# Optimization experiments

Measured on AMD Instinct MI355X. Metric: run time of the kernel, lower is better.

The kernel has to match this reference:

```python
import jax, jax.numpy as jnp
import numpy as np

N_NODES = 65536
N_EDGES = N_NODES * 16
NEG_SLOPE = 0.2


def setup_inputs() -> dict:
    key = jax.random.key(0)
    ks = jax.random.split(key, 32)
    x = jax.random.normal(ks[0], (N_NODES, 336), dtype=jnp.float32)
    ei = jax.random.randint(ks[1], (2, N_EDGES), 0, N_NODES)
    src, dst = ei[0], ei[1]
    dst = jnp.where(src == dst, (dst + 1) % N_NODES, dst)  # no pre-existing self-loops
    edge_index = jnp.stack([src, dst])
    batch = jnp.arange(N_NODES) // 8

    def mk(k, shape, fan_in):
        return jax.random.normal(k, shape, dtype=jnp.float32) * (1.0 / np.sqrt(fan_in))

    conv_dims = [(336, 125), (250, 75), (150, 50), (100, 30)]
    H = 2
    p = {}
    ki = 2
    for i, (cin, cout) in enumerate(conv_dims, 1):
        p[f"W{i}"] = mk(ks[ki], (cin, H * cout), cin); ki += 1
        p[f"as{i}"] = mk(ks[ki], (H, cout), cout); ki += 1
        p[f"ad{i}"] = mk(ks[ki], (H, cout), cout); ki += 1
        p[f"b{i}"] = jnp.zeros((H * cout,), dtype=jnp.float32)
    lin_dims = [(480, 200), (200, 100), (100, 100), (100, 29)]
    for i, (cin, cout) in enumerate(lin_dims, 1):
        p[f"lw{i}"] = mk(ks[ki], (cin, cout), cin); ki += 1
        p[f"lb{i}"] = jnp.zeros((cout,), dtype=jnp.float32)
    return {"x": x, "edge_index": edge_index, "batch": batch, **p}


def gat_conv(x, src, dst, W, a_src, a_dst, bias):
    # PyG GATConv (concat=True): gather -> LeakyReLU score -> segment softmax over dst -> scatter-add
    N = x.shape[0]
    H, C = a_src.shape
    h = (x @ W).reshape(N, H, C)                      # [N,H,C]
    al_s = jnp.sum(h * a_src, axis=-1)                # [N,H]
    al_d = jnp.sum(h * a_dst, axis=-1)
    e = jax.nn.leaky_relu(al_s[src] + al_d[dst], NEG_SLOPE)  # [E,H]
    m = jax.ops.segment_max(e, dst, num_segments=N)   # [N,H]
    m = jnp.where(jnp.isfinite(m), m, 0.0)
    ex = jnp.exp(e - m[dst])
    den = jax.ops.segment_sum(ex, dst, num_segments=N)
    alpha = ex / den[dst]                             # [E,H]
    out = jax.ops.segment_sum(alpha[:, :, None] * h[src], dst, num_segments=N)
    return out.reshape(N, H * C) + bias


def reference(x, edge_index, batch,
              W1, as1, ad1, b1, W2, as2, ad2, b2,
              W3, as3, ad3, b3, W4, as4, ad4, b4,
              lw1, lb1, lw2, lb2, lw3, lb3, lw4, lb4):
    N = x.shape[0]
    loops = jnp.arange(N)
    src = jnp.concatenate([edge_index[0], loops])  # add self-loops (PyG default)
    dst = jnp.concatenate([edge_index[1], loops])
    h = jax.nn.relu(gat_conv(x, src, dst, W1, as1, ad1, b1))
    h = jax.nn.relu(gat_conv(h, src, dst, W2, as2, ad2, b2))
    h = jax.nn.relu(gat_conv(h, src, dst, W3, as3, ad3, b3))
    h = jax.nn.relu(gat_conv(h, src, dst, W4, as4, ad4, b4))
    h = h.reshape(-1, 480)                         # 8 nodes per graph * 60 feats
    h = jax.nn.relu(h @ lw1 + lb1)
    h = jax.nn.relu(h @ lw2 + lb2)
    h = jax.nn.relu(h @ lw3 + lb3)
    return h @ lw4 + lb4
```

## Files before the change

kernel.cpp:

```cpp
#include <hip/hip_runtime.h>
#include <hip/hip_bf16.h>
#include <stdint.h>

#define N_NODES 65536
#define N_EDGES (N_NODES * 16)
#define NEG_SLOPE 0.2f

typedef short bf16x8 __attribute__((ext_vector_type(8)));
typedef float f32x4 __attribute__((ext_vector_type(4)));
typedef unsigned int u32x2 __attribute__((ext_vector_type(2)));
typedef _Float16 f16x4 __attribute__((ext_vector_type(4)));

__device__ __forceinline__ unsigned short f2bf(float f) {
    unsigned u = __float_as_uint(f);
    u += 0x7fffu + ((u >> 16) & 1u);
    return (unsigned short)(u >> 16);
}
__device__ __forceinline__ float bf2f(unsigned short h) {
    return __uint_as_float(((unsigned)h) << 16);
}
__device__ __forceinline__ unsigned short f2h(float f) {
    _Float16 h = (_Float16)f;
    union { _Float16 h; unsigned short u; } cv; cv.h = h; return cv.u;
}
__device__ __forceinline__ float rl_f(float v, int lane) {
    return __int_as_float(__builtin_amdgcn_readlane(__float_as_int(v), lane));
}
__device__ __forceinline__ void load_lds16(const void* g, void* l) {
    __builtin_amdgcn_global_load_lds(
        (const __attribute__((address_space(1))) unsigned int*)g,
        (__attribute__((address_space(3))) unsigned int*)l, 16, 0, 0);
}
__device__ __forceinline__ void nt_store_us4(unsigned short* p, ushort4 v) {
    u32x2 d;
    d.x = (unsigned)v.x | ((unsigned)v.y << 16);
    d.y = (unsigned)v.z | ((unsigned)v.w << 16);
    __builtin_nontemporal_store(d, (u32x2*)p);
}

template<int TN>
__global__ __launch_bounds__(256) void gemm_mfma(
    const float* __restrict__ A32, int KA,
    const unsigned short* __restrict__ Ahi, const unsigned short* __restrict__ Alo,
    int lda, int Kp,
    const unsigned short* __restrict__ Bhi, const unsigned short* __restrict__ Blo,
    unsigned short* __restrict__ C16,
    int ldc, int Nw,
    const float* __restrict__ asrc, const float* __restrict__ adst,
    float* __restrict__ alS, float* __restrict__ alD, int Cal, int HCal)
{
    constexpr int NI = TN / 32;
    __shared__ unsigned short sAhi[128 * 32], sAlo[128 * 32];
    __shared__ unsigned short sBhi[TN * 32],  sBlo[TN * 32];
    __shared__ float sAl[128][2][4];
    const int tid = threadIdx.x;
    const int wave = tid >> 6, lane = tid & 63;
    const int row0 = blockIdx.y * 128;
    const int col0 = blockIdx.x * TN;
    const int wm = (wave & 1) * 64, wn = (wave >> 1) * (TN / 2);
    const int mlane = lane & 15, q = lane >> 4;

    f32x4 acc[4][NI];
#pragma unroll
    for (int a = 0; a < 4; ++a)
#pragma unroll
        for (int b = 0; b < NI; ++b) acc[a][b] = (f32x4){0.f, 0.f, 0.f, 0.f};

    for (int k0 = 0; k0 < Kp; k0 += 32) {
        __syncthreads();
        if (A32) {
            const int r = tid >> 1, cbase = (tid & 1) * 16;
            const float* Ap = A32 + (size_t)(row0 + r) * lda;
#pragma unroll
            for (int j = 0; j < 4; ++j) {
                int kc = k0 + cbase + j * 4;
                float4 v = make_float4(0.f, 0.f, 0.f, 0.f);
                if (kc < KA) v = *(const float4*)(Ap + kc);
                ushort4 h, l;
                h.x = f2bf(v.x); l.x = f2bf(v.x - bf2f(h.x));
                h.y = f2bf(v.y); l.y = f2bf(v.y - bf2f(h.y));
                h.z = f2bf(v.z); l.z = f2bf(v.z - bf2f(h.z));
                h.w = f2bf(v.w); l.w = f2bf(v.w - bf2f(h.w));
                *(ushort4*)(sAhi + r * 32 + cbase + j * 4) = h;
                *(ushort4*)(sAlo + r * 32 + cbase + j * 4) = l;
            }
        } else {
#pragma unroll
            for (int cc = 0; cc < 2; ++cc) {
                int c = wave * 2 + cc;
                int r = c * 16 + (lane >> 2);
                size_t goff = (size_t)(row0 + r) * lda + k0 + (lane & 3) * 8;
                load_lds16(Ahi + goff, sAhi + c * 512);
                load_lds16(Alo + goff, sAlo + c * 512);
            }
        }
        {
#pragma unroll
            for (int cc = 0; cc < TN / 64; ++cc) {
                int c = wave * (TN / 64) + cc;
                int r = c * 16 + (lane >> 2);
                size_t goff = (size_t)(col0 + r) * Kp + k0 + (lane & 3) * 8;
                load_lds16(Bhi + goff, sBhi + c * 512);
                load_lds16(Blo + goff, sBlo + c * 512);
            }
        }
        __syncthreads();

        bf16x8 ah[4], al[4], bh[NI], bl[NI];
#pragma unroll
        for (int mi = 0; mi < 4; ++mi) {
            int m = wm + mi * 16 + mlane;
            ah[mi] = *(const bf16x8*)(sAhi + m * 32 + q * 8);
            al[mi] = *(const bf16x8*)(sAlo + m * 32 + q * 8);
        }
#pragma unroll
        for (int ni = 0; ni < NI; ++ni) {
            int n = wn + ni * 16 + mlane;
            bh[ni] = *(const bf16x8*)(sBhi + n * 32 + q * 8);
            bl[ni] = *(const bf16x8*)(sBlo + n * 32 + q * 8);
        }
#pragma unroll
        for (int mi = 0; mi < 4; ++mi)
#pragma unroll
            for (int ni = 0; ni < NI; ++ni) {
                acc[mi][ni] = __builtin_amdgcn_mfma_f32_16x16x32_bf16(ah[mi], bh[ni], acc[mi][ni], 0, 0, 0);
                acc[mi][ni] = __builtin_amdgcn_mfma_f32_16x16x32_bf16(al[mi], bh[ni], acc[mi][ni], 0, 0, 0);
                acc[mi][ni] = __builtin_amdgcn_mfma_f32_16x16x32_bf16(ah[mi], bl[ni], acc[mi][ni], 0, 0, 0);
            }
    }

#pragma unroll
    for (int ni = 0; ni < NI; ++ni) {
        int col = col0 + wn + ni * 16 + mlane;
        if (col >= Nw) continue;
#pragma unroll
        for (int mi = 0; mi < 4; ++mi) {
#pragma unroll
            for (int reg = 0; reg < 4; ++reg) {
                int row = row0 + wm + mi * 16 + q * 4 + reg;
                C16[(size_t)row * ldc + col] = f2h(acc[mi][ni][reg]);
            }
        }
    }

    if (asrc) {
        float asv[NI], adv[NI];
        bool head0[NI];
#pragma unroll
        for (int ni = 0; ni < NI; ++ni) {
            int col = col0 + wn + ni * 16 + mlane;
            bool valid = col < HCal;
            head0[ni] = col < Cal;
            asv[ni] = valid ? asrc[col] : 0.f;
            adv[ni] = valid ? adst[col] : 0.f;
        }
#pragma unroll
        for (int mi = 0; mi < 4; ++mi) {
#pragma unroll
            for (int reg = 0; reg < 4; ++reg) {
                float s0 = 0.f, s1 = 0.f, d0 = 0.f, d1 = 0.f;
#pragma unroll
                for (int ni = 0; ni < NI; ++ni) {
                    float v = acc[mi][ni][reg];
                    if (head0[ni]) { s0 += v * asv[ni]; d0 += v * adv[ni]; }
                    else           { s1 += v * asv[ni]; d1 += v * adv[ni]; }
                }
#pragma unroll
                for (int off = 1; off < 16; off <<= 1) {
                    s0 += __shfl_xor(s0, off); s1 += __shfl_xor(s1, off);
                    d0 += __shfl_xor(d0, off); d1 += __shfl_xor(d1, off);
                }
                if (mlane == 0) {
                    int rl = wm + mi * 16 + q * 4 + reg;
                    int slot = wave >> 1;
                    sAl[rl][slot][0] = s0; sAl[rl][slot][1] = s1;
                    sAl[rl][slot][2] = d0; sAl[rl][slot][3] = d1;
                }
            }
        }
        __syncthreads();
        if (tid < 128) {
            int row = row0 + tid;
            float v0 = sAl[tid][0][0] + sAl[tid][1][0];
            float v1 = sAl[tid][0][1] + sAl[tid][1][1];
            float v2 = sAl[tid][0][2] + sAl[tid][1][2];
            float v3 = sAl[tid][0][3] + sAl[tid][1][3];
            atomicAdd(&alS[row * 2 + 0], v0);
            atomicAdd(&alS[row * 2 + 1], v1);
            atomicAdd(&alD[row * 2 + 0], v2);
            atomicAdd(&alD[row * 2 + 1], v3);
        }
    }
}

template<int NI>
__device__ __forceinline__ void mlp_layer(
    const unsigned short* aHi, const unsigned short* aLo, int ldaS, int K,
    const unsigned short* __restrict__ Bhi, const unsigned short* __restrict__ Blo,
    int Kp,
    unsigned short* sBh, unsigned short* sBl,
    const float* __restrict__ bias, int Nbias, int colBase,
    unsigned short* oHi, unsigned short* oLo, int ldo, int Nstore,
    float* __restrict__ gOut, int row0, int relu,
    int wave, int lane)
{
    const int mlane = lane & 15, q = lane >> 4;
    const int wm = (wave & 1) * 16;
    const int wn = (wave >> 1) * (NI * 16);
    f32x4 acc[NI];
#pragma unroll
    for (int b = 0; b < NI; ++b) acc[b] = (f32x4){0.f, 0.f, 0.f, 0.f};

    for (int k0 = 0; k0 < K; k0 += 32) {
        __syncthreads();
        for (int c = wave; c < NI * 2; c += 4) {
            int r = c * 16 + (lane >> 2);
            size_t goff = (size_t)r * Kp + k0 + (lane & 3) * 8;
            load_lds16(Bhi + goff, sBh + c * 512);
            load_lds16(Blo + goff, sBl + c * 512);
        }
        __syncthreads();

        bf16x8 ah, al, bh[NI], bl[NI];
        ah = *(const bf16x8*)(aHi + (wm + mlane) * ldaS + k0 + q * 8);
        al = *(const bf16x8*)(aLo + (wm + mlane) * ldaS + k0 + q * 8);
#pragma unroll
        for (int ni = 0; ni < NI; ++ni) {
            int n = wn + ni * 16 + mlane;
            bh[ni] = *(const bf16x8*)(sBh + n * 32 + q * 8);
            bl[ni] = *(const bf16x8*)(sBl + n * 32 + q * 8);
        }
#pragma unroll
        for (int ni = 0; ni < NI; ++ni) {
            acc[ni] = __builtin_amdgcn_mfma_f32_16x16x32_bf16(ah, bh[ni], acc[ni], 0, 0, 0);
            acc[ni] = __builtin_amdgcn_mfma_f32_16x16x32_bf16(al, bh[ni], acc[ni], 0, 0, 0);
            acc[ni] = __builtin_amdgcn_mfma_f32_16x16x32_bf16(ah, bl[ni], acc[ni], 0, 0, 0);
        }
    }
    __syncthreads();

#pragma unroll
    for (int ni = 0; ni < NI; ++ni) {
        int colg = colBase + wn + ni * 16 + mlane;
        float bv = (colg < Nbias) ? bias[colg] : 0.f;
#pragma unroll
        for (int reg = 0; reg < 4; ++reg) {
            int row = wm + q * 4 + reg;
            float v = acc[ni][reg] + bv;
            if (relu) v = fmaxf(v, 0.f);
            if (gOut) {
                if (colg < 29) gOut[(size_t)(row0 + row) * 29 + colg] = v;
            } else if (colg < Nstore) {
                unsigned short h = f2bf(v);
                oHi[row * ldo + colg] = h;
                oLo[row * ldo + colg] = f2bf(v - bf2f(h));
            }
        }
    }
}

__global__ __launch_bounds__(256) void mlp_fused(
    const unsigned short* __restrict__ actHi, const unsigned short* __restrict__ actLo,
    const unsigned short* __restrict__ L1h, const unsigned short* __restrict__ L1l,
    const unsigned short* __restrict__ L2h, const unsigned short* __restrict__ L2l,
    const unsigned short* __restrict__ L3h, const unsigned short* __restrict__ L3l,
    const unsigned short* __restrict__ L4h, const unsigned short* __restrict__ L4l,
    const float* __restrict__ B1, const float* __restrict__ B2,
    const float* __restrict__ B3, const float* __restrict__ B4,
    float* __restrict__ out)
{
    __shared__ unsigned short b1h[32 * 224], b1l[32 * 224];
    __shared__ unsigned short b2h[32 * 128], b2l[32 * 128];
    __shared__ unsigned short sAh[32 * 32],  sAl[32 * 32];
    __shared__ unsigned short sBh[128 * 32], sBl[128 * 32];
    const int tid = threadIdx.x;
    const int wave = tid >> 6, lane = tid & 63;
    const int row0 = blockIdx.x * 32;
    const int mlane = lane & 15, q = lane >> 4;
    const int wm = (wave & 1) * 16;
    const int wn = (wave >> 1) * 64;

    for (int nt = 0; nt < 2; ++nt) {
        const unsigned short* Bh = L1h + (size_t)nt * 128 * 512;
        const unsigned short* Bl = L1l + (size_t)nt * 128 * 512;
        f32x4 acc[4];
#pragma unroll
        for (int b = 0; b < 4; ++b) acc[b] = (f32x4){0.f, 0.f, 0.f, 0.f};
        for (int k0 = 0; k0 < 512; k0 += 32) {
            __syncthreads();
            for (int c = wave; c < 2; c += 4) {
                int r = c * 16 + (lane >> 2);
                size_t goff = (size_t)(row0 + r) * 512 + k0 + (lane & 3) * 8;
                load_lds16(actHi + goff, sAh + c * 512);
                load_lds16(actLo + goff, sAl + c * 512);
            }
            for (int c = wave; c < 8; c += 4) {
                int r = c * 16 + (lane >> 2);
                size_t goff = (size_t)r * 512 + k0 + (lane & 3) * 8;
                load_lds16(Bh + goff, sBh + c * 512);
                load_lds16(Bl + goff, sBl + c * 512);
            }
            __syncthreads();
            bf16x8 ah = *(const bf16x8*)(sAh + (wm + mlane) * 32 + q * 8);
            bf16x8 al = *(const bf16x8*)(sAl + (wm + mlane) * 32 + q * 8);
#pragma unroll
            for (int ni = 0; ni < 4; ++ni) {
                int n = wn + ni * 16 + mlane;
                bf16x8 bh = *(const bf16x8*)(sBh + n * 32 + q * 8);
                bf16x8 bl = *(const bf16x8*)(sBl + n * 32 + q * 8);
                acc[ni] = __builtin_amdgcn_mfma_f32_16x16x32_bf16(ah, bh, acc[ni], 0, 0, 0);
                acc[ni] = __builtin_amdgcn_mfma_f32_16x16x32_bf16(al, bh, acc[ni], 0, 0, 0);
                acc[ni] = __builtin_amdgcn_mfma_f32_16x16x32_bf16(ah, bl, acc[ni], 0, 0, 0);
            }
        }
        __syncthreads();
#pragma unroll
        for (int ni = 0; ni < 4; ++ni) {
            int colg = nt * 128 + wn + ni * 16 + mlane;
            float bv = (colg < 200) ? B1[colg] : 0.f;
#pragma unroll
            for (int reg = 0; reg < 4; ++reg) {
                int row = wm + q * 4 + reg;
                float v = fmaxf(acc[ni][reg] + bv, 0.f);
                if (colg < 224) {
                    unsigned short h = f2bf(v);
                    b1h[row * 224 + colg] = h;
                    b1l[row * 224 + colg] = f2bf(v - bf2f(h));
                }
            }
        }
    }
    __syncthreads();

    mlp_layer<4>(b1h, b1l, 224, 224, L2h, L2l, 224, sBh, sBl,
                 B2, 100, 0, b2h, b2l, 128, 128, nullptr, 0, 1, wave, lane);
    __syncthreads();
    mlp_layer<4>(b2h, b2l, 128, 128, L3h, L3l, 128, sBh, sBl,
                 B3, 100, 0, b1h, b1l, 128, 128, nullptr, 0, 1, wave, lane);
    __syncthreads();
    mlp_layer<2>(b1h, b1l, 128, 128, L4h, L4l, 128, sBh, sBl,
                 B4, 29, 0, nullptr, nullptr, 0, 0, out, row0, 0, wave, lane);
}

struct WtJob {
    const float* W; unsigned short* Whi; unsigned short* Wlo;
    int K, N, Kp, remap, nb0;
};
struct WtJobs { WtJob j[8]; };

__global__ void wt_decomp_all(WtJobs jobs)
{
    int b = blockIdx.x;
    int idx = 0;
#pragma unroll
    for (int i = 1; i < 8; ++i)
        if (b >= jobs.j[i].nb0) idx = i;
    WtJob jb = jobs.j[idx];
    int n = b - jb.nb0;
    for (int k = threadIdx.x; k < jb.Kp; k += 256) {
        int ks = k, valid = 1;
        if (jb.remap) {
            int bb = k >> 6, r = k & 63;
            if (r < 60) ks = bb * 60 + r; else valid = 0;
        }
        float v = 0.f;
        if (valid && ks < jb.K && n < jb.N) v = jb.W[(size_t)ks * jb.N + n];
        unsigned short h = f2bf(v);
        jb.Whi[(size_t)n * jb.Kp + k] = h;
        jb.Wlo[(size_t)n * jb.Kp + k] = f2bf(v - bf2f(h));
    }
}

template<int LPE>
__global__ __launch_bounds__(256) void gat_gather_fused(
    const unsigned short* __restrict__ h16,
    const float* __restrict__ al_s, const float* __restrict__ al_d,
    const int* __restrict__ indptr, const unsigned short* __restrict__ csr_src,
    const float* __restrict__ bias,
    unsigned short* __restrict__ outHi, unsigned short* __restrict__ outLo,
    int ldo, int Nn, int C, int HC, int HCpad)
{
    constexpr int G = 64 / LPE;
    const int wave = threadIdx.x >> 6, lane = threadIdx.x & 63;
    const int i = blockIdx.x * 4 + wave;
    if (i >= Nn) return;
    const int start = indptr[i], end = indptr[i + 1];
    const int deg = end - start;
    const float ad0 = al_d[2 * i], ad1 = al_d[2 * i + 1];

    const int l = lane % LPE;
    const int g = lane / LPE;
    const int ch4 = l * 4;
    const bool chA = ch4 < HCpad;
    const bool c0 = (ch4 + 0) < C, c1 = (ch4 + 1) < C,
               c2 = (ch4 + 2) < C, c3 = (ch4 + 3) < C;
    float a0 = 0.f, a1 = 0.f, a2 = 0.f, a3 = 0.f;

    if (deg <= 64) {
        const int jW = start + lane;
        const bool have = jW < end;
        int ps = 0;
        float e0r = 0.f, e1r = 0.f;
        if (have) {
            ps = csr_src[jW];
            float2 as = *(const float2*)(al_s + 2 * ps);
            e0r = as.x + ad0; e0r = e0r > 0.f ? e0r : NEG_SLOPE * e0r;
            e1r = as.y + ad1; e1r = e1r > 0.f ? e1r : NEG_SLOPE * e1r;
        }
        float m0 = have ? e0r : -1e30f;
        float m1 = have ? e1r : -1e30f;
#pragma unroll
        for (int off = 32; off; off >>= 1) {
            m0 = fmaxf(m0, __shfl_xor(m0, off));
            m1 = fmaxf(m1, __shfl_xor(m1, off));
        }
        float n0 = have ? __expf(e0r - m0) : 0.f;
        float n1 = have ? __expf(e1r - m1) : 0.f;
        float den0 = n0, den1 = n1;
#pragma unroll
        for (int off = 32; off; off >>= 1) {
            den0 += __shfl_xor(den0, off);
            den1 += __shfl_xor(den1, off);
        }
        const float pw0 = n0 * (1.f / den0);
        const float pw1 = n1 * (1.f / den1);

        if constexpr (G == 1) {
            for (int u = 0; u < deg; ++u) {
                float w0 = rl_f(pw0, u);
                float w1 = rl_f(pw1, u);
                int s = __builtin_amdgcn_readlane(ps, u);
                float hx = 0.f, hy = 0.f, hz = 0.f, hw = 0.f;
                if (chA) {
                    f16x4 hv = *(const f16x4*)(h16 + (size_t)s * HCpad + ch4);
                    hx = (float)hv[0]; hy = (float)hv[1];
                    hz = (float)hv[2]; hw = (float)hv[3];
                }
                a0 = fmaf(c0 ? w0 : w1, hx, a0);
                a1 = fmaf(c1 ? w0 : w1, hy, a1);
                a2 = fmaf(c2 ? w0 : w1, hz, a2);
                a3 = fmaf(c3 ? w0 : w1, hw, a3);
            }
        } else {
            const int nit = (deg + G - 1) / G;
            for (int u = 0; u < nit; ++u) {
                int idx = u * G + g;
                float w0 = __shfl(pw0, idx);
                float w1 = __shfl(pw1, idx);
                int s = __shfl(ps, idx);
                float hx = 0.f, hy = 0.f, hz = 0.f, hw = 0.f;
                if (chA) {
                    f16x4 hv = *(const f16x4*)(h16 + (size_t)s * HCpad + ch4);
                    hx = (float)hv[0]; hy = (float)hv[1];
                    hz = (float)hv[2]; hw = (float)hv[3];
                }
                a0 = fmaf(c0 ? w0 : w1, hx, a0);
                a1 = fmaf(c1 ? w0 : w1, hy, a1);
                a2 = fmaf(c2 ? w0 : w1, hz, a2);
                a3 = fmaf(c3 ? w0 : w1, hw, a3);
            }
        }
    } else {
        float m0 = -1e30f, m1 = -1e30f, den0 = 0.f, den1 = 0.f;
        for (int j = start + lane; j < end; j += 64) {
            int s = csr_src[j];
            float2 as = *(const float2*)(al_s + 2 * s);
            float e0 = as.x + ad0; e0 = e0 > 0.f ? e0 : NEG_SLOPE * e0;
            float e1 = as.y + ad1; e1 = e1 > 0.f ? e1 : NEG_SLOPE * e1;
            float n0 = fmaxf(m0, e0);
            den0 = den0 * __expf(m0 - n0) + __expf(e0 - n0);
            m0 = n0;
            float n1 = fmaxf(m1, e1);
            den1 = den1 * __expf(m1 - n1) + __expf(e1 - n1);
            m1 = n1;
        }
#pragma unroll
        for (int off = 32; off; off >>= 1) {
            float mo0 = __shfl_xor(m0, off), do0 = __shfl_xor(den0, off);
            float n0 = fmaxf(m0, mo0);
            den0 = den0 * __expf(m0 - n0) + do0 * __expf(mo0 - n0);
            m0 = n0;
            float mo1 = __shfl_xor(m1, off), do1 = __shfl_xor(den1, off);
            float n1 = fmaxf(m1, mo1);
            den1 = den1 * __expf(m1 - n1) + do1 * __expf(mo1 - n1);
            m1 = n1;
        }
        const float inv0 = 1.f / den0, inv1 = 1.f / den1;

        for (int jb = start; jb < end; jb += 64) {
            int jW = jb + lane;
            float pw0 = 0.f, pw1 = 0.f;
            int ps = 0;
            if (jW < end) {
                ps = csr_src[jW];
                float2 as = *(const float2*)(al_s + 2 * ps);
                float e0 = as.x + ad0; e0 = e0 > 0.f ? e0 : NEG_SLOPE * e0;
                float e1 = as.y + ad1; e1 = e1 > 0.f ? e1 : NEG_SLOPE * e1;
                pw0 = __expf(e0 - m0) * inv0;
                pw1 = __expf(e1 - m1) * inv1;
            }
            int nedge = end - jb; if (nedge > 64) nedge = 64;
            int nit = (nedge + G - 1) / G;
            for (int u = 0; u < nit; ++u) {
                int idx = u * G + g;
                float w0 = __shfl(pw0, idx);
                float w1 = __shfl(pw1, idx);
                int s = __shfl(ps, idx);
                float hx = 0.f, hy = 0.f, hz = 0.f, hw = 0.f;
                if (chA) {
                    f16x4 hv = *(const f16x4*)(h16 + (size_t)s * HCpad + ch4);
                    hx = (float)hv[0]; hy = (float)hv[1];
                    hz = (float)hv[2]; hw = (float)hv[3];
                }
                a0 = fmaf(c0 ? w0 : w1, hx, a0);
                a1 = fmaf(c1 ? w0 : w1, hy, a1);
                a2 = fmaf(c2 ? w0 : w1, hz, a2);
                a3 = fmaf(c3 ? w0 : w1, hw, a3);
            }
        }
    }

#pragma unroll
    for (int off = LPE; off < 64; off <<= 1) {
        a0 += __shfl_xor(a0, off);
        a1 += __shfl_xor(a1, off);
        a2 += __shfl_xor(a2, off);
        a3 += __shfl_xor(a3, off);
    }
    if (g == 0 && chA) {
        float bx = (ch4 + 0 < HC) ? bias[ch4 + 0] : 0.f;
        float by = (ch4 + 1 < HC) ? bias[ch4 + 1] : 0.f;
        float bz = (ch4 + 2 < HC) ? bias[ch4 + 2] : 0.f;
        float bw = (ch4 + 3 < HC) ? bias[ch4 + 3] : 0.f;
        float v0 = fmaxf(a0 + bx, 0.f);
        float v1 = fmaxf(a1 + by, 0.f);
        float v2 = fmaxf(a2 + bz, 0.f);
        float v3 = fmaxf(a3 + bw, 0.f);
        ushort4 h, lo;
        h.x = f2bf(v0); lo.x = f2bf(v0 - bf2f(h.x));
        h.y = f2bf(v1); lo.y = f2bf(v1 - bf2f(h.y));
        h.z = f2bf(v2); lo.z = f2bf(v2 - bf2f(h.z));
        h.w = f2bf(v3); lo.w = f2bf(v3 - bf2f(h.w));
        nt_store_us4(outHi + (size_t)i * ldo + ch4, h);
        nt_store_us4(outLo + (size_t)i * ldo + ch4, lo);
    }
    for (int z = HCpad + lane * 4; z < ldo; z += 256) {
        ushort4 zz; zz.x = zz.y = zz.z = zz.w = 0;
        *(ushort4*)(outHi + (size_t)i * ldo + z) = zz;
        *(ushort4*)(outLo + (size_t)i * ldo + z) = zz;
    }
}

__global__ void hist_self_k(const int* __restrict__ dst, int E,
                            int* __restrict__ counts, int n)
{
    int gid = blockIdx.x * blockDim.x + threadIdx.x;
    if (gid < E) atomicAdd(&counts[dst[gid]], 1);
    else if (gid < E + n) atomicAdd(&counts[gid - E], 1);
}

__global__ void scan_block_k(const int* __restrict__ in, int* __restrict__ out,
                             int* __restrict__ bsum, int n)
{
    __shared__ int sh[256];
    int gid = blockIdx.x * 256 + threadIdx.x;
    int v = (gid < n) ? in[gid] : 0;
    sh[threadIdx.x] = v;
    __syncthreads();
    for (int off = 1; off < 256; off <<= 1) {
        int t = (threadIdx.x >= off) ? sh[threadIdx.x - off] : 0;
        __syncthreads();
        sh[threadIdx.x] += t;
        __syncthreads();
    }
    int incl = sh[threadIdx.x];
    if (gid < n) out[gid] = incl - v;
    if (threadIdx.x == 255) bsum[blockIdx.x] = incl;
}

__global__ void scan_tops_k(const int* __restrict__ bsum, int* __restrict__ boff)
{
    __shared__ int sh[256];
    int v = bsum[threadIdx.x];
    sh[threadIdx.x] = v;
    __syncthreads();
    for (int off = 1; off < 256; off <<= 1) {
        int t = (threadIdx.x >= off) ? sh[threadIdx.x - off] : 0;
        __syncthreads();
        sh[threadIdx.x] += t;
        __syncthreads();
    }
    boff[threadIdx.x] = sh[threadIdx.x] - v;
}

__global__ void scan_add_k(int* __restrict__ indptr, const int* __restrict__ boff,
                           int n, int Etot)
{
    int gid = blockIdx.x * 256 + threadIdx.x;
    if (gid < n) indptr[gid] += boff[blockIdx.x];
    if (gid == 0) indptr[n] = Etot;
}

__global__ void fill_all_k(const int* __restrict__ src, const int* __restrict__ dst,
                           int E, const int* __restrict__ indptr,
                           int* __restrict__ cursor,
                           unsigned short* __restrict__ csr_src, int n)
{
    int gid = blockIdx.x * blockDim.x + threadIdx.x;
    if (gid < E) {
        int d = dst[gid];
        int pos = atomicAdd(&cursor[d], 1);
        csr_src[indptr[d] + pos] = (unsigned short)src[gid];
    } else if (gid < E + n) {
        int i = gid - E;
        int pos = atomicAdd(&cursor[i], 1);
        csr_src[indptr[i] + pos] = (unsigned short)i;
    }
}

extern "C" void kernel_launch(void* const* d_in, const int* in_sizes, int n_in,
                              void* d_out, int out_size, void* d_ws, size_t ws_size,
                              hipStream_t stream)
{
    (void)in_sizes; (void)n_in; (void)out_size; (void)ws_size;
    const int N = N_NODES;
    const int E = N_EDGES;
    const int Etot = E + N;

    const float* x = (const float*)d_in[0];
    const int* ei = (const int*)d_in[1];
    const float* Wc[4] = {(const float*)d_in[3], (const float*)d_in[7],
                          (const float*)d_in[11], (const float*)d_in[15]};
    const float* AS[4] = {(const float*)d_in[4], (const float*)d_in[8],
                          (const float*)d_in[12], (const float*)d_in[16]};
    const float* AD[4] = {(const float*)d_in[5], (const float*)d_in[9],
                          (const float*)d_in[13], (const float*)d_in[17]};
    const float* Bc[4] = {(const float*)d_in[6], (const float*)d_in[10],
                          (const float*)d_in[14], (const float*)d_in[18]};
    const float* LW[4] = {(const float*)d_in[19], (const float*)d_in[21],
                          (const float*)d_in[23], (const float*)d_in[25]};
    const float* LB[4] = {(const float*)d_in[20], (const float*)d_in[22],
                          (const float*)d_in[24], (const float*)d_in[26]};

    char* w = (char*)d_ws;
    auto alloc = [&](size_t bytes) -> char* {
        char* p = w; w += (bytes + 255) & ~(size_t)255; return p;
    };
    unsigned short* bufC16 = (unsigned short*)alloc((size_t)N * 256 * 2);
    unsigned short* actHi = (unsigned short*)alloc((size_t)N * 256 * 2);
    unsigned short* actLo = (unsigned short*)alloc((size_t)N * 256 * 2);
    unsigned short* csr = (unsigned short*)alloc((size_t)Etot * 2);
    float* alSD = (float*)alloc((size_t)N * 4 * 4 * 4 + (size_t)N * 2 * 4);
    int* cnt2   = (int*)(alSD + (size_t)N * 16);
    int* counts = cnt2;
    int* cursor = cnt2 + N;
    int* indptr = (int*)alloc((size_t)(N + 8) * 4);
    int* bsum   = (int*)alloc(1024);
    int* boff   = (int*)alloc(1024);

    const int KpConv[4] = {352, 256, 160, 128};
    const int NpConv[4] = {256, 192, 128, 64};
    const int KpLin[4]  = {512, 224, 128, 128};
    const int NpLin[4]  = {256, 128, 128, 64};
    unsigned short *WtHi[4], *WtLo[4], *LtHi[4], *LtLo[4];
    for (int l = 0; l < 4; ++l) {
        WtHi[l] = (unsigned short*)alloc((size_t)NpConv[l] * KpConv[l] * 2);
        WtLo[l] = (unsigned short*)alloc((size_t)NpConv[l] * KpConv[l] * 2);
    }
    for (int l = 0; l < 4; ++l) {
        LtHi[l] = (unsigned short*)alloc((size_t)NpLin[l] * KpLin[l] * 2);
        LtLo[l] = (unsigned short*)alloc((size_t)NpLin[l] * KpLin[l] * 2);
    }

    const int* esrc = ei;
    const int* edst = ei + E;

    hipMemsetAsync(alSD, 0, (size_t)N * 4 * 4 * 4 + (size_t)N * 2 * 4, stream);
    hist_self_k<<<(E + N) / 256, 256, 0, stream>>>(edst, E, counts, N);
    scan_block_k<<<N / 256, 256, 0, stream>>>(counts, indptr, bsum, N);
    scan_tops_k<<<1, 256, 0, stream>>>(bsum, boff);
    scan_add_k<<<N / 256, 256, 0, stream>>>(indptr, boff, N, Etot);
    fill_all_k<<<(E + N) / 256, 256, 0, stream>>>(esrc, edst, E, indptr, cursor, csr, N);

    const int Kc[4] = {336, 250, 150, 100}, Nc[4] = {250, 150, 100, 60};
    const int Kl[4] = {480, 200, 100, 100}, Nl[4] = {200, 100, 100, 29};
    WtJobs jobs;
    int nb = 0;
    for (int l = 0; l < 4; ++l) {
        jobs.j[l] = {Wc[l], WtHi[l], WtLo[l], Kc[l], Nc[l], KpConv[l], 0, nb};
        nb += NpConv[l];
    }
    for (int l = 0; l < 4; ++l) {
        jobs.j[4 + l] = {LW[l], LtHi[l], LtLo[l], Kl[l], Nl[l], KpLin[l],
                         l == 0 ? 1 : 0, nb};
        nb += NpLin[l];
    }
    wt_decomp_all<<<nb, 256, 0, stream>>>(jobs);

    const int HCp[4]  = {256, 152, 100, 60};
    const int ldoA[4] = {256, 160, 128, 64};
    const int ldaA[4] = {336, 256, 160, 128};
    for (int l = 0; l < 4; ++l) {
        int C = Nc[l] / 2, HC = Nc[l];
        float* alS = alSD + (size_t)l * N * 4;
        float* alD = alS + (size_t)N * 2;
        if (l == 0) {
            gemm_mfma<128><<<dim3(2, N / 128), 256, 0, stream>>>(
                x, 336, nullptr, nullptr, 336, 352,
                WtHi[0], WtLo[0],
                bufC16, HCp[0], HCp[0],
                AS[0], AD[0], alS, alD, C, HC);
        } else if (l == 1) {
            gemm_mfma<64><<<dim3(3, N / 128), 256, 0, stream>>>(
                nullptr, 0, actHi, actLo, ldaA[1], KpConv[1],
                WtHi[1], WtLo[1],
                bufC16, HCp[1], HCp[1],
                AS[1], AD[1], alS, alD, C, HC);
        } else if (l == 2) {
            gemm_mfma<128><<<dim3(1, N / 128), 256, 0, stream>>>(
                nullptr, 0, actHi, actLo, ldaA[2], KpConv[2],
                WtHi[2], WtLo[2],
                bufC16, HCp[2], HCp[2],
                AS[2], AD[2], alS, alD, C, HC);
        } else {
            gemm_mfma<64><<<dim3(1, N / 128), 256, 0, stream>>>(
                nullptr, 0, actHi, actLo, ldaA[3], KpConv[3],
                WtHi[3], WtLo[3],
                bufC16, HCp[3], HCp[3],
                AS[3], AD[3], alS, alD, C, HC);
        }
        if (l == 0) {
            gat_gather_fused<64><<<N / 4, 256, 0, stream>>>(
                bufC16, alS, alD, indptr, csr, Bc[0],
                actHi, actLo, ldoA[0], N, C, HC, HCp[0]);
        } else if (l == 1) {
            gat_gather_fused<64><<<N / 4, 256, 0, stream>>>(
                bufC16, alS, alD, indptr, csr, Bc[1],
                actHi, actLo, ldoA[1], N, C, HC, HCp[1]);
        } else if (l == 2) {
            gat_gather_fused<32><<<N / 4, 256, 0, stream>>>(
                bufC16, alS, alD, indptr, csr, Bc[2],
                actHi, actLo, ldoA[2], N, C, HC, HCp[2]);
        } else {
            gat_gather_fused<16><<<N / 4, 256, 0, stream>>>(
                bufC16, alS, alD, indptr, csr, Bc[3],
                actHi, actLo, ldoA[3], N, C, HC, HCp[3]);
        }
    }

    mlp_fused<<<8192 / 32, 256, 0, stream>>>(
        actHi, actLo,
        LtHi[0], LtLo[0], LtHi[1], LtLo[1],
        LtHi[2], LtLo[2], LtHi[3], LtLo[3],
        LB[0], LB[1], LB[2], LB[3],
        (float*)d_out);
}
```

Measured before the change: 813.3 us.

## Pad each attention head to aligned column blocks and unroll gather loops

Each head's channels are now laid out in a padded block (e.g. 125→128), and the weight-decomposition kernel remaps weight rows and columns to match. With this layout every 4-channel group in the gather kernel belongs to a single head, so one weight select replaces four per-element selects. The edge loops are rounded up to a multiple of four and unrolled by four, relying on zero weights for the padded edges. This adds index-remapping logic and slightly wider padded buffers, and leans on the padded entries reading as zero.

New measurement: 838.1 us. +3.0%, slower.

```diff
diff --git a/kernel.cpp b/kernel.cpp
--- a/kernel.cpp
+++ b/kernel.cpp
@@ -47,7 +47,7 @@
     unsigned short* __restrict__ C16,
     int ldc, int Nw,
     const float* __restrict__ asrc, const float* __restrict__ adst,
-    float* __restrict__ alS, float* __restrict__ alD, int Cal, int HCal)
+    float* __restrict__ alS, float* __restrict__ alD, int Cal, int Pal)
 {
     constexpr int NI = TN / 32;
     __shared__ unsigned short sAhi[128 * 32], sAlo[128 * 32];
@@ -149,10 +149,13 @@
 #pragma unroll
         for (int ni = 0; ni < NI; ++ni) {
             int col = col0 + wn + ni * 16 + mlane;
-            bool valid = col < HCal;
-            head0[ni] = col < Cal;
-            asv[ni] = valid ? asrc[col] : 0.f;
-            adv[ni] = valid ? adst[col] : 0.f;
+            int hd = col >= Pal;
+            int idc = hd ? col - Pal : col;
+            bool valid = idc < Cal;
+            head0[ni] = !hd;
+            int borig = hd ? Cal + idc : idc;
+            asv[ni] = valid ? asrc[borig] : 0.f;
+            adv[ni] = valid ? adst[borig] : 0.f;
         }
 #pragma unroll
         for (int mi = 0; mi < 4; ++mi) {
@@ -344,7 +347,7 @@
 
 struct WtJob {
     const float* W; unsigned short* Whi; unsigned short* Wlo;
-    int K, N, Kp, remap, nb0;
+    int N, Kp, K, nb0, Cn, Pn, Ck, Pk, kblk;
 };
 struct WtJobs { WtJob j[8]; };
 
@@ -357,14 +360,30 @@
         if (b >= jobs.j[i].nb0) idx = i;
     WtJob jb = jobs.j[idx];
     int n = b - jb.nb0;
+    int norig = n; bool nvalid;
+    if (jb.Pn) {
+        int hn = n >= jb.Pn;
+        int r = hn ? n - jb.Pn : n;
+        nvalid = r < jb.Cn;
+        norig = hn ? jb.Cn + r : r;
+    } else {
+        nvalid = n < jb.N;
+    }
     for (int k = threadIdx.x; k < jb.Kp; k += 256) {
-        int ks = k, valid = 1;
-        if (jb.remap) {
-            int bb = k >> 6, r = k & 63;
-            if (r < 60) ks = bb * 60 + r; else valid = 0;
+        int ks; bool kvalid;
+        if (jb.Pk) {
+            int node = k / jb.kblk;
+            int r = k - node * jb.kblk;
+            int rr, off;
+            if (r < jb.Pk) { rr = r; off = 0; kvalid = rr < jb.Ck; }
+            else if (r < 2 * jb.Pk) { rr = r - jb.Pk; off = jb.Ck; kvalid = rr < jb.Ck; }
+            else { rr = 0; off = 0; kvalid = false; }
+            ks = node * (2 * jb.Ck) + off + rr;
+        } else {
+            ks = k; kvalid = k < jb.K;
         }
         float v = 0.f;
-        if (valid && ks < jb.K && n < jb.N) v = jb.W[(size_t)ks * jb.N + n];
+        if (nvalid && kvalid) v = jb.W[(size_t)ks * jb.N + norig];
         unsigned short h = f2bf(v);
         jb.Whi[(size_t)n * jb.Kp + k] = h;
         jb.Wlo[(size_t)n * jb.Kp + k] = f2bf(v - bf2f(h));
@@ -378,7 +397,7 @@
     const int* __restrict__ indptr, const unsigned short* __restrict__ csr_src,
     const float* __restrict__ bias,
     unsigned short* __restrict__ outHi, unsigned short* __restrict__ outLo,
-    int ldo, int Nn, int C, int HC, int HCpad)
+    int ldo, int Nn, int C, int P, int HCpad)
 {
     constexpr int G = 64 / LPE;
     const int wave = threadIdx.x >> 6, lane = threadIdx.x & 63;
@@ -392,8 +411,7 @@
     const int g = lane / LPE;
     const int ch4 = l * 4;
     const bool chA = ch4 < HCpad;
-    const bool c0 = (ch4 + 0) < C, c1 = (ch4 + 1) < C,
-               c2 = (ch4 + 2) < C, c3 = (ch4 + 3) < C;
+    const bool hd1 = ch4 >= P;
     float a0 = 0.f, a1 = 0.f, a2 = 0.f, a3 = 0.f;
 
     if (deg <= 64) {
@@ -426,9 +444,12 @@
         const float pw1 = n1 * (1.f / den1);
 
         if constexpr (G == 1) {
-            for (int u = 0; u < deg; ++u) {
+            const int dr = (deg + 3) & ~3;
+#pragma unroll 4
+            for (int u = 0; u < dr; ++u) {
                 float w0 = rl_f(pw0, u);
                 float w1 = rl_f(pw1, u);
+                float w = hd1 ? w1 : w0;
                 int s = __builtin_amdgcn_readlane(ps, u);
                 float hx = 0.f, hy = 0.f, hz = 0.f, hw = 0.f;
                 if (chA) {
@@ -436,17 +457,20 @@
                     hx = (float)hv[0]; hy = (float)hv[1];
                     hz = (float)hv[2]; hw = (float)hv[3];
                 }
-                a0 = fmaf(c0 ? w0 : w1, hx, a0);
-                a1 = fmaf(c1 ? w0 : w1, hy, a1);
-                a2 = fmaf(c2 ? w0 : w1, hz, a2);
-                a3 = fmaf(c3 ? w0 : w1, hw, a3);
+                a0 = fmaf(w, hx, a0);
+                a1 = fmaf(w, hy, a1);
+                a2 = fmaf(w, hz, a2);
+                a3 = fmaf(w, hw, a3);
             }
         } else {
             const int nit = (deg + G - 1) / G;
-            for (int u = 0; u < nit; ++u) {
+            const int nit4 = (nit + 3) & ~3;
+#pragma unroll 4
+            for (int u = 0; u < nit4; ++u) {
                 int idx = u * G + g;
                 float w0 = __shfl(pw0, idx);
                 float w1 = __shfl(pw1, idx);
+                float w = hd1 ? w1 : w0;
                 int s = __shfl(ps, idx);
                 float hx = 0.f, hy = 0.f, hz = 0.f, hw = 0.f;
                 if (chA) {
@@ -454,10 +478,10 @@
                     hx = (float)hv[0]; hy = (float)hv[1];
                     hz = (float)hv[2]; hw = (float)hv[3];
                 }
-                a0 = fmaf(c0 ? w0 : w1, hx, a0);
-                a1 = fmaf(c1 ? w0 : w1, hy, a1);
-                a2 = fmaf(c2 ? w0 : w1, hz, a2);
-                a3 = fmaf(c3 ? w0 : w1, hw, a3);
+                a0 = fmaf(w, hx, a0);
+                a1 = fmaf(w, hy, a1);
+                a2 = fmaf(w, hz, a2);
+                a3 = fmaf(w, hw, a3);
             }
         }
     } else {
@@ -505,6 +529,7 @@
                 int idx = u * G + g;
                 float w0 = __shfl(pw0, idx);
                 float w1 = __shfl(pw1, idx);
+                float w = hd1 ? w1 : w0;
                 int s = __shfl(ps, idx);
                 float hx = 0.f, hy = 0.f, hz = 0.f, hw = 0.f;
                 if (chA) {
@@ -512,10 +537,10 @@
                     hx = (float)hv[0]; hy = (float)hv[1];
                     hz = (float)hv[2]; hw = (float)hv[3];
                 }
-                a0 = fmaf(c0 ? w0 : w1, hx, a0);
-                a1 = fmaf(c1 ? w0 : w1, hy, a1);
-                a2 = fmaf(c2 ? w0 : w1, hz, a2);
-                a3 = fmaf(c3 ? w0 : w1, hw, a3);
+                a0 = fmaf(w, hx, a0);
+                a1 = fmaf(w, hy, a1);
+                a2 = fmaf(w, hz, a2);
+                a3 = fmaf(w, hw, a3);
             }
         }
     }
@@ -528,19 +553,21 @@
         a3 += __shfl_xor(a3, off);
     }
     if (g == 0 && chA) {
-        float bx = (ch4 + 0 < HC) ? bias[ch4 + 0] : 0.f;
-        float by = (ch4 + 1 < HC) ? bias[ch4 + 1] : 0.f;
-        float bz = (ch4 + 2 < HC) ? bias[ch4 + 2] : 0.f;
-        float bw = (ch4 + 3 < HC) ? bias[ch4 + 3] : 0.f;
-        float v0 = fmaxf(a0 + bx, 0.f);
-        float v1 = fmaxf(a1 + by, 0.f);
-        float v2 = fmaxf(a2 + bz, 0.f);
-        float v3 = fmaxf(a3 + bw, 0.f);
-        ushort4 h, lo;
-        h.x = f2bf(v0); lo.x = f2bf(v0 - bf2f(h.x));
-        h.y = f2bf(v1); lo.y = f2bf(v1 - bf2f(h.y));
-        h.z = f2bf(v2); lo.z = f2bf(v2 - bf2f(h.z));
-        h.w = f2bf(v3); lo.w = f2bf(v3 - bf2f(h.w));
+        float av[4] = {a0, a1, a2, a3};
+        unsigned short hi4[4], lo4[4];
+#pragma unroll
+        for (int k = 0; k < 4; ++k) {
+            int colp = ch4 + k;
+            int idc = hd1 ? colp - P : colp;
+            bool vld = idc < C;
+            float bv = vld ? bias[hd1 ? C + idc : idc] : 0.f;
+            float v = vld ? fmaxf(av[k] + bv, 0.f) : 0.f;
+            unsigned short h = f2bf(v);
+            hi4[k] = h;
+            lo4[k] = f2bf(v - bf2f(h));
+        }
+        ushort4 h = {hi4[0], hi4[1], hi4[2], hi4[3]};
+        ushort4 lo = {lo4[0], lo4[1], lo4[2], lo4[3]};
         nt_store_us4(outHi + (size_t)i * ldo + ch4, h);
         nt_store_us4(outLo + (size_t)i * ldo + ch4, lo);
     }
@@ -682,26 +709,39 @@
     scan_add_k<<<N / 256, 256, 0, stream>>>(indptr, boff, N, Etot);
     fill_all_k<<<(E + N) / 256, 256, 0, stream>>>(esrc, edst, E, indptr, cursor, csr, N);
 
-    const int Kc[4] = {336, 250, 150, 100}, Nc[4] = {250, 150, 100, 60};
-    const int Kl[4] = {480, 200, 100, 100}, Nl[4] = {200, 100, 100, 29};
+    const int Cc[4] = {125, 75, 50, 30};
+    const int Pc[4] = {128, 76, 52, 32};
+    const int Nc[4] = {250, 150, 100, 60};
+    const int Kl[4] = {480, 200, 100, 100};
+    const int Nl[4] = {200, 100, 100, 29};
     WtJobs jobs;
     int nb = 0;
     for (int l = 0; l < 4; ++l) {
-        jobs.j[l] = {Wc[l], WtHi[l], WtLo[l], Kc[l], Nc[l], KpConv[l], 0, nb};
+        WtJob jb;
+        jb.W = Wc[l]; jb.Whi = WtHi[l]; jb.Wlo = WtLo[l];
+        jb.N = Nc[l]; jb.Kp = KpConv[l]; jb.nb0 = nb;
+        jb.Cn = Cc[l]; jb.Pn = Pc[l];
+        if (l == 0) { jb.Pk = 0; jb.Ck = 0; jb.kblk = 1; jb.K = 336; }
+        else { jb.Pk = Pc[l-1]; jb.Ck = Cc[l-1]; jb.kblk = KpConv[l]; jb.K = 0; }
+        jobs.j[l] = jb;
         nb += NpConv[l];
     }
     for (int l = 0; l < 4; ++l) {
-        jobs.j[4 + l] = {LW[l], LtHi[l], LtLo[l], Kl[l], Nl[l], KpLin[l],
-                         l == 0 ? 1 : 0, nb};
+        WtJob jb;
+        jb.W = LW[l]; jb.Whi = LtHi[l]; jb.Wlo = LtLo[l];
+        jb.N = Nl[l]; jb.Kp = KpLin[l]; jb.nb0 = nb;
+        jb.Cn = 0; jb.Pn = 0;
+        if (l == 0) { jb.Pk = Pc[3]; jb.Ck = Cc[3]; jb.kblk = 64; jb.K = 0; }
+        else { jb.Pk = 0; jb.Ck = 0; jb.kblk = 1; jb.K = Kl[l]; }
+        jobs.j[4 + l] = jb;
         nb += NpLin[l];
     }
     wt_decomp_all<<<nb, 256, 0, stream>>>(jobs);
 
-    const int HCp[4]  = {256, 152, 100, 60};
+    const int HCp[4]  = {256, 152, 104, 64};
     const int ldoA[4] = {256, 160, 128, 64};
     const int ldaA[4] = {336, 256, 160, 128};
     for (int l = 0; l < 4; ++l) {
-        int C = Nc[l] / 2, HC = Nc[l];
         float* alS = alSD + (size_t)l * N * 4;
         float* alD = alS + (size_t)N * 2;
         if (l == 0) {
@@ -709,42 +749,42 @@
                 x, 336, nullptr, nullptr, 336, 352,
                 WtHi[0], WtLo[0],
                 bufC16, HCp[0], HCp[0],
-                AS[0], AD[0], alS, alD, C, HC);
+                AS[0], AD[0], alS, alD, Cc[0], Pc[0]);
         } else if (l == 1) {
             gemm_mfma<64><<<dim3(3, N / 128), 256, 0, stream>>>(
                 nullptr, 0, actHi, actLo, ldaA[1], KpConv[1],
                 WtHi[1], WtLo[1],
                 bufC16, HCp[1], HCp[1],
-                AS[1], AD[1], alS, alD, C, HC);
+                AS[1], AD[1], alS, alD, Cc[1], Pc[1]);
         } else if (l == 2) {
             gemm_mfma<128><<<dim3(1, N / 128), 256, 0, stream>>>(
                 nullptr, 0, actHi, actLo, ldaA[2], KpConv[2],
                 WtHi[2], WtLo[2],
                 bufC16, HCp[2], HCp[2],
-                AS[2], AD[2], alS, alD, C, HC);
+                AS[2], AD[2], alS, alD, Cc[2], Pc[2]);
         } else {
             gemm_mfma<64><<<dim3(1, N / 128), 256, 0, stream>>>(
                 nullptr, 0, actHi, actLo, ldaA[3], KpConv[3],
                 WtHi[3], WtLo[3],
                 bufC16, HCp[3], HCp[3],
-                AS[3], AD[3], alS, alD, C, HC);
+                AS[3], AD[3], alS, alD, Cc[3], Pc[3]);
         }
         if (l == 0) {
             gat_gather_fused<64><<<N / 4, 256, 0, stream>>>(
                 bufC16, alS, alD, indptr, csr, Bc[0],
-                actHi, actLo, ldoA[0], N, C, HC, HCp[0]);
+                actHi, actLo, ldoA[0], N, Cc[0], Pc[0], HCp[0]);
         } else if (l == 1) {
             gat_gather_fused<64><<<N / 4, 256, 0, stream>>>(
                 bufC16, alS, alD, indptr, csr, Bc[1],
-                actHi, actLo, ldoA[1], N, C, HC, HCp[1]);
+                actHi, actLo, ldoA[1], N, Cc[1], Pc[1], HCp[1]);
         } else if (l == 2) {
             gat_gather_fused<32><<<N / 4, 256, 0, stream>>>(
                 bufC16, alS, alD, indptr, csr, Bc[2],
-                actHi, actLo, ldoA[2], N, C, HC, HCp[2]);
+                actHi, actLo, ldoA[2], N, Cc[2], Pc[2], HCp[2]);
         } else {
             gat_gather_fused<16><<<N / 4, 256, 0, stream>>>(
                 bufC16, alS, alD, indptr, csr, Bc[3],
-                actHi, actLo, ldoA[3], N, C, HC, HCp[3]);
+                actHi, actLo, ldoA[3], N, Cc[3], Pc[3], HCp[3]);
         }
     }
 
```
